# Kernel optimization log

Measured on AMD Instinct MI355X. Metric: run time of the kernel, lower is better.

## Reference

```python
import jax, jax.numpy as jnp
import numpy as np

B, N, F, D, H = 4, 2048, 128, 128, 4

def setup_inputs() -> dict:
    key = jax.random.key(0)
    k1, k2, k3, k4 = jax.random.split(key, 4)
    X = jax.random.normal(k1, (B, N, F), dtype=jnp.float32)
    A = jax.random.uniform(k2, (B, N, N), dtype=jnp.float32)
    kernel = jax.random.normal(k3, (F, D), dtype=jnp.float32) * 0.05
    bias = jnp.ones((D,), dtype=jnp.float32)
    attn = jax.random.normal(k4, (H, D, D), dtype=jnp.float32) * 0.05
    return {"X": X, "A": A, "kernel": kernel, "bias": bias, "attn": attn}

def reference(X, A, kernel, bias, attn):
    # Linear projection: [B,N,F] @ [F,D] + bias -> [B,N,D]
    Xp = jnp.einsum('bnf,fd->bnd', X, kernel) + bias
    # Per-head bilinear scores Xp @ attn_h @ Xp^T, batched over heads: [B,H,N,N]
    scores = jnp.einsum('bnd,hde,bme->bhnm', Xp, attn, Xp)
    # Adjacency mask + tanh (fused elementwise)
    Am = jnp.tanh(A[:, None, :, :] * scores)
    # Weighted aggregate per head: [B,H,N,N] @ [B,N,D] -> [B,H,N,D]
    heads = jnp.einsum('bhnm,bmd->bhnd', Am, Xp)
    # Mean over heads, relu
    Xh = jax.nn.relu(jnp.mean(heads, axis=1))
    # Skip connection (shapes match since F == D): relu(Xh + X)
    out = jax.nn.relu(Xh + X)
    return out
```

## Files before the change

### kernel.cpp

```cpp
#include <hip/hip_runtime.h>

#define NB 4
#define NN 2048
#define ND 128
#define NH 4

typedef short short8 __attribute__((ext_vector_type(8)));
typedef short short4v __attribute__((ext_vector_type(4)));
typedef float floatx4 __attribute__((ext_vector_type(4)));

__device__ __forceinline__ short f2bf(float f){
  unsigned u = __float_as_uint(f);
  u += 0x7FFFu + ((u >> 16) & 1u);
  return (short)(u >> 16);
}
__device__ __forceinline__ float bf2f(short s){
  unsigned u = ((unsigned)(unsigned short)s) << 16;
  return __uint_as_float(u);
}

__global__ void k0_transpose(const float* __restrict__ W, const float* __restrict__ attn,
                             short* __restrict__ WT, short* __restrict__ attnT){
  int mat = blockIdx.x;
  const float* src = (mat == 0) ? W : (attn + (mat - 1) * 16384);
  short* dst = (mat == 0) ? WT : (attnT + (mat - 1) * 16384);
  __shared__ short tile[128 * 130];
  int t = threadIdx.x;
  for (int k = 0; k < 64; ++k){
    int idx = k * 256 + t;
    int r = idx >> 7, c = idx & 127;
    tile[c * 130 + r] = f2bf(src[idx]);
  }
  __syncthreads();
  for (int k = 0; k < 8; ++k){
    int g = k * 256 + t;
    int r = g >> 4, c8 = g & 15;
    short8 v;
    #pragma unroll
    for (int j = 0; j < 8; ++j) v[j] = tile[r * 130 + c8 * 8 + j];
    *(short8*)&dst[r * 128 + c8 * 8] = v;
  }
}

__global__ __launch_bounds__(256) void k1_xp(const float* __restrict__ X,
                                             const short* __restrict__ WT,
                                             const float* __restrict__ bias,
                                             short* __restrict__ Xp){
  int bid = blockIdx.x;
  int b = bid >> 5, i0 = (bid & 31) << 6;
  int t = threadIdx.x, w = t >> 6, lane = t & 63, lq = lane >> 4, lc = lane & 15;
  __shared__ __align__(16) short ldsB[16384];
  #pragma unroll
  for (int c = 0; c < 8; ++c){
    int q = c * 256 + t; int fblk = q >> 7; int d = q & 127;
    *(short8*)&ldsB[q * 8] = *(const short8*)&WT[d * 128 + fblk * 8];
  }
  short8 af[4][4];
  #pragma unroll
  for (int ib = 0; ib < 4; ++ib)
    #pragma unroll
    for (int k = 0; k < 4; ++k){
      const float* xp = &X[(b * NN + i0 + ib * 16 + lc) * ND + k * 32 + lq * 8];
      float4 x0 = *(const float4*)xp;
      float4 x1 = *(const float4*)(xp + 4);
      short8 s;
      s[0]=f2bf(x0.x); s[1]=f2bf(x0.y); s[2]=f2bf(x0.z); s[3]=f2bf(x0.w);
      s[4]=f2bf(x1.x); s[5]=f2bf(x1.y); s[6]=f2bf(x1.z); s[7]=f2bf(x1.w);
      af[ib][k] = s;
    }
  __syncthreads();
  floatx4 acc[4][2];
  #pragma unroll
  for (int ib = 0; ib < 4; ++ib)
    #pragma unroll
    for (int eb = 0; eb < 2; ++eb) acc[ib][eb] = (floatx4){0.f, 0.f, 0.f, 0.f};
  #pragma unroll
  for (int eb = 0; eb < 2; ++eb)
    #pragma unroll
    for (int k = 0; k < 4; ++k){
      short8 bf = *(short8*)&ldsB[(k * 4 + lq) * 1024 + (w * 32 + eb * 16 + lc) * 8];
      #pragma unroll
      for (int ib = 0; ib < 4; ++ib)
        acc[ib][eb] = __builtin_amdgcn_mfma_f32_16x16x32_bf16(af[ib][k], bf, acc[ib][eb], 0, 0, 0);
    }
  #pragma unroll
  for (int ib = 0; ib < 4; ++ib)
    #pragma unroll
    for (int eb = 0; eb < 2; ++eb){
      int d = w * 32 + eb * 16 + lc;
      float bv = bias[d];
      #pragma unroll
      for (int r = 0; r < 4; ++r){
        int n = i0 + ib * 16 + lq * 4 + r;
        Xp[(b * NN + n) * ND + d] = f2bf(acc[ib][eb][r] + bv);
      }
    }
}

__global__ void k1b_transpose(const short* __restrict__ Xp, short* __restrict__ XpT){
  int bid = blockIdx.x;
  int b = bid >> 6; int rem = bid & 63;
  int n0 = (rem >> 1) << 6, d0 = (rem & 1) << 6;
  __shared__ short tile[64 * 66];
  int t = threadIdx.x;
  #pragma unroll
  for (int c = 0; c < 2; ++c){
    int g = c * 256 + t; int r = g >> 3, c8 = g & 7;
    short8 v = *(const short8*)&Xp[(b * NN + n0 + r) * ND + d0 + c8 * 8];
    #pragma unroll
    for (int j = 0; j < 8; ++j) tile[(c8 * 8 + j) * 66 + r] = v[j];
  }
  __syncthreads();
  #pragma unroll
  for (int c = 0; c < 2; ++c){
    int g = c * 256 + t; int d = g >> 3, n8 = g & 7;
    short8 v;
    #pragma unroll
    for (int j = 0; j < 8; ++j) v[j] = tile[d * 66 + n8 * 8 + j];
    *(short8*)&XpT[(b * ND + d0 + d) * NN + n0 + n8 * 8] = v;
  }
}

__global__ __launch_bounds__(256) void k2_y(const short* __restrict__ Xp,
                                            const short* __restrict__ attnT,
                                            short* __restrict__ Y){
  int bid = blockIdx.x;
  int it = bid & 31, h = (bid >> 5) & 3, b = bid >> 7;
  int i0 = it << 6;
  int t = threadIdx.x, w = t >> 6, lane = t & 63, lq = lane >> 4, lc = lane & 15;
  __shared__ __align__(16) short ldsB[16384];
  const short* Bsrc = attnT + h * 16384;
  #pragma unroll
  for (int c = 0; c < 8; ++c){
    int q = c * 256 + t; int dblk = q >> 7; int e = q & 127;
    *(short8*)&ldsB[q * 8] = *(const short8*)&Bsrc[e * 128 + dblk * 8];
  }
  short8 af[4][4];
  #pragma unroll
  for (int ib = 0; ib < 4; ++ib)
    #pragma unroll
    for (int k = 0; k < 4; ++k)
      af[ib][k] = *(const short8*)&Xp[(b * NN + i0 + ib * 16 + lc) * ND + k * 32 + lq * 8];
  __syncthreads();
  floatx4 acc[4][2];
  #pragma unroll
  for (int ib = 0; ib < 4; ++ib)
    #pragma unroll
    for (int eb = 0; eb < 2; ++eb) acc[ib][eb] = (floatx4){0.f, 0.f, 0.f, 0.f};
  #pragma unroll
  for (int eb = 0; eb < 2; ++eb)
    #pragma unroll
    for (int k = 0; k < 4; ++k){
      short8 bf = *(short8*)&ldsB[(k * 4 + lq) * 1024 + (w * 32 + eb * 16 + lc) * 8];
      #pragma unroll
      for (int ib = 0; ib < 4; ++ib)
        acc[ib][eb] = __builtin_amdgcn_mfma_f32_16x16x32_bf16(af[ib][k], bf, acc[ib][eb], 0, 0, 0);
    }
  #pragma unroll
  for (int ib = 0; ib < 4; ++ib)
    #pragma unroll
    for (int eb = 0; eb < 2; ++eb){
      int e = w * 32 + eb * 16 + lc;
      #pragma unroll
      for (int r = 0; r < 4; ++r){
        int n = i0 + ib * 16 + lq * 4 + r;
        Y[((b * NH + h) * NN + n) * ND + e] = f2bf(acc[ib][eb][r]);
      }
    }
}

__global__ __launch_bounds__(256, 3) void k3_fused(const short* __restrict__ Xp,
                                                   const short* __restrict__ XpT,
                                                   const short* __restrict__ Y,
                                                   const float* __restrict__ A,
                                                   float* __restrict__ part){
  int bid = blockIdx.x;
  int it = bid & 127, b = (bid >> 7) & 3, ms = bid >> 9;
  int i0 = it << 4;
  int t = threadIdx.x, w = t >> 6, lane = t & 63, lq = lane >> 4, lc = lane & 15;

  __shared__ __align__(16) short ldsPh[2][1024];
  __shared__ __align__(16) short ldsPl[2][1024];

  short8 yf[4][4];
  #pragma unroll
  for (int h = 0; h < 4; ++h)
    #pragma unroll
    for (int k = 0; k < 4; ++k)
      yf[h][k] = *(const short8*)&Y[((b * NH + h) * NN + i0 + lc) * ND + k * 32 + lq * 8];

  floatx4 acc[2];
  acc[0] = (floatx4){0.f,0.f,0.f,0.f};
  acc[1] = (floatx4){0.f,0.f,0.f,0.f};

  const int mbase = ms << 9;
  const int poff = (w * 2 + (lq >> 1)) * 128 + lc * 8 + (lq & 1) * 4;

  const short* xr  = Xp  + (size_t)(b * NN + mbase + w * 16 + lc) * ND;
  const short* pvB = XpT + (size_t)(b * ND + w * 32 + lc) * NN + mbase;
  const float* Ar  = A   + (size_t)(b * NN + i0 + lc) * NN + mbase + w * 16 + lq * 4;

  short8 xpf_c[4];
  #pragma unroll
  for (int k = 0; k < 4; ++k) xpf_c[k] = *(const short8*)&xr[k * 32 + lq * 8];
  floatx4 av_c = *(const floatx4*)Ar;

  for (int itn = 0; itn < 8; ++itn){
    int p = itn & 1;
    short8 pvb[2][2];
    #pragma unroll
    for (int kb = 0; kb < 2; ++kb)
      #pragma unroll
      for (int db = 0; db < 2; ++db)
        pvb[kb][db] = *(const short8*)&pvB[(size_t)(db * 16) * NN + kb * 32 + lq * 8];

    float av2[4];
    #pragma unroll
    for (int r = 0; r < 4; ++r) av2[r] = av_c[r] * 2.885390081777926f;
    float rs[4] = {0.f, 0.f, 0.f, 0.f};
    #pragma unroll
    for (int h = 0; h < 4; ++h){
      floatx4 S = (floatx4){0.f,0.f,0.f,0.f};
      #pragma unroll
      for (int k = 0; k < 4; ++k)
        S = __builtin_amdgcn_mfma_f32_16x16x32_bf16(xpf_c[k], yf[h][k], S, 0, 0, 0);
      #pragma unroll
      for (int r = 0; r < 4; ++r){
        float e = __builtin_amdgcn_exp2f(av2[r] * S[r]);
        rs[r] += __builtin_amdgcn_rcpf(e + 1.f);
      }
    }

    int adv = (itn < 7) ? 64 : 0;
    xr += (size_t)adv * ND; Ar += adv; 
    short8 xpf_n[4];
    #pragma unroll
    for (int k = 0; k < 4; ++k) xpf_n[k] = *(const short8*)&xr[k * 32 + lq * 8];
    floatx4 av_n = *(const floatx4*)Ar;

    short4v hi4, lo4;
    #pragma unroll
    for (int r = 0; r < 4; ++r){
      float pb = 1.f - 0.5f * rs[r];
      short h16 = f2bf(pb);
      hi4[r] = h16;
      lo4[r] = f2bf(pb - bf2f(h16));
    }
    *(short4v*)&ldsPh[p][poff] = hi4;
    *(short4v*)&ldsPl[p][poff] = lo4;

    asm volatile("s_waitcnt lgkmcnt(0)\n\ts_barrier" ::: "memory");

    #pragma unroll
    for (int kb = 0; kb < 2; ++kb){
      short8 ph = *(short8*)&ldsPh[p][(kb * 4 + lq) * 128 + lc * 8];
      short8 pl = *(short8*)&ldsPl[p][(kb * 4 + lq) * 128 + lc * 8];
      #pragma unroll
      for (int db = 0; db < 2; ++db){
        acc[db] = __builtin_amdgcn_mfma_f32_16x16x32_bf16(ph, pvb[kb][db], acc[db], 0, 0, 0);
        acc[db] = __builtin_amdgcn_mfma_f32_16x16x32_bf16(pl, pvb[kb][db], acc[db], 0, 0, 0);
      }
    }
    pvB += adv;
    #pragma unroll
    for (int k = 0; k < 4; ++k) xpf_c[k] = xpf_n[k];
    av_c = av_n;
  }
  float* dst = part + (size_t)ms * 1048576 + (b * NN + i0) * ND;
  #pragma unroll
  for (int db = 0; db < 2; ++db)
    #pragma unroll
    for (int r = 0; r < 4; ++r)
      dst[(lq * 4 + r) * ND + w * 32 + db * 16 + lc] = acc[db][r];
}

__global__ void k4_final(const float* __restrict__ part, const float* __restrict__ X,
                         float* __restrict__ out){
  int f = (blockIdx.x * 256 + threadIdx.x) * 4;
  float4 s0 = *(const float4*)(part + f);
  float4 s1 = *(const float4*)(part + 1048576 + f);
  float4 s2 = *(const float4*)(part + 2097152 + f);
  float4 s3 = *(const float4*)(part + 3145728 + f);
  float4 xv = *(const float4*)(X + f);
  float4 o;
  o.x = fmaxf(fmaxf(s0.x + s1.x + s2.x + s3.x, 0.f) + xv.x, 0.f);
  o.y = fmaxf(fmaxf(s0.y + s1.y + s2.y + s3.y, 0.f) + xv.y, 0.f);
  o.z = fmaxf(fmaxf(s0.z + s1.z + s2.z + s3.z, 0.f) + xv.z, 0.f);
  o.w = fmaxf(fmaxf(s0.w + s1.w + s2.w + s3.w, 0.f) + xv.w, 0.f);
  *(float4*)(out + f) = o;
}

extern "C" void kernel_launch(void* const* d_in, const int* in_sizes, int n_in,
                              void* d_out, int out_size, void* d_ws, size_t ws_size,
                              hipStream_t stream) {
  const float* X    = (const float*)d_in[0];
  const float* A    = (const float*)d_in[1];
  const float* W    = (const float*)d_in[2];
  const float* bias = (const float*)d_in[3];
  const float* attn = (const float*)d_in[4];
  float* out = (float*)d_out;

  const size_t OFF_XP    = 0;
  const size_t OFF_XPT   = (size_t)2 << 20;
  const size_t OFF_Y     = (size_t)4 << 20;
  const size_t OFF_PART  = (size_t)12 << 20;
  const size_t OFF_WT    = (size_t)28 << 20;
  const size_t OFF_ATTNT = OFF_WT + 32768;
  const size_t NEED = OFF_ATTNT + 131072;
  if (ws_size < NEED) return;

  char* ws = (char*)d_ws;
  short* Xp    = (short*)(ws + OFF_XP);
  short* XpT   = (short*)(ws + OFF_XPT);
  short* Y     = (short*)(ws + OFF_Y);
  float* part  = (float*)(ws + OFF_PART);
  short* WT    = (short*)(ws + OFF_WT);
  short* attnT = (short*)(ws + OFF_ATTNT);

  k0_transpose<<<5, 256, 0, stream>>>(W, attn, WT, attnT);
  k1_xp<<<128, 256, 0, stream>>>(X, WT, bias, Xp);
  k1b_transpose<<<256, 256, 0, stream>>>(Xp, XpT);
  k2_y<<<512, 256, 0, stream>>>(Xp, attnT, Y);
  k3_fused<<<2048, 256, 0, stream>>>(Xp, XpT, Y, A, part);
  k4_final<<<1024, 256, 0, stream>>>(part, X, out);
}
```

Measured before the change: 196.5 us.

## Fuse Xp transpose into projection; restructure aggregation with bpermute and per-wave full-D tiles

The projection kernel now stages its bias-added output in LDS and writes both Xp and its transpose, so the separate transpose launch goes away. The fused attention kernel now has each wave compute all 128 output columns for its own key slice. It shuffles the hi/lo bf16 probability fragments across lanes with ds_bpermute instead of LDS plus a per-iteration barrier. Wave partials are then reduced once through LDS at the end, and the M range is split in two instead of four, which halves the partial buffers read by the final kernel. In exchange, each thread holds more accumulator and B-fragment registers, which may lower occupancy, and half as many blocks are launched.

```diff
diff --git a/kernel.cpp b/kernel.cpp
--- a/kernel.cpp
+++ b/kernel.cpp
@@ -6,7 +6,6 @@
 #define NH 4
 
 typedef short short8 __attribute__((ext_vector_type(8)));
-typedef short short4v __attribute__((ext_vector_type(4)));
 typedef float floatx4 __attribute__((ext_vector_type(4)));
 
 __device__ __forceinline__ short f2bf(float f){
@@ -17,6 +16,9 @@
 __device__ __forceinline__ float bf2f(short s){
   unsigned u = ((unsigned)(unsigned short)s) << 16;
   return __uint_as_float(u);
+}
+__device__ __forceinline__ int pack2(short lo, short hi){
+  return ((int)(unsigned short)hi << 16) | (int)(unsigned short)lo;
 }
 
 __global__ void k0_transpose(const float* __restrict__ W, const float* __restrict__ attn,
@@ -45,7 +47,8 @@
 __global__ __launch_bounds__(256) void k1_xp(const float* __restrict__ X,
                                              const short* __restrict__ WT,
                                              const float* __restrict__ bias,
-                                             short* __restrict__ Xp){
+                                             short* __restrict__ Xp,
+                                             short* __restrict__ XpT){
   int bid = blockIdx.x;
   int b = bid >> 5, i0 = (bid & 31) << 6;
   int t = threadIdx.x, w = t >> 6, lane = t & 63, lq = lane >> 4, lc = lane & 15;
@@ -83,6 +86,7 @@
       for (int ib = 0; ib < 4; ++ib)
         acc[ib][eb] = __builtin_amdgcn_mfma_f32_16x16x32_bf16(af[ib][k], bf, acc[ib][eb], 0, 0, 0);
     }
+  __syncthreads();
   #pragma unroll
   for (int ib = 0; ib < 4; ++ib)
     #pragma unroll
@@ -91,33 +95,24 @@
       float bv = bias[d];
       #pragma unroll
       for (int r = 0; r < 4; ++r){
-        int n = i0 + ib * 16 + lq * 4 + r;
-        Xp[(b * NN + n) * ND + d] = f2bf(acc[ib][eb][r] + bv);
+        int n = ib * 16 + lq * 4 + r;
+        ldsB[d * 72 + n] = f2bf(acc[ib][eb][r] + bv);
       }
     }
-}
-
-__global__ void k1b_transpose(const short* __restrict__ Xp, short* __restrict__ XpT){
-  int bid = blockIdx.x;
-  int b = bid >> 6; int rem = bid & 63;
-  int n0 = (rem >> 1) << 6, d0 = (rem & 1) << 6;
-  __shared__ short tile[64 * 66];
-  int t = threadIdx.x;
-  #pragma unroll
-  for (int c = 0; c < 2; ++c){
-    int g = c * 256 + t; int r = g >> 3, c8 = g & 7;
-    short8 v = *(const short8*)&Xp[(b * NN + n0 + r) * ND + d0 + c8 * 8];
-    #pragma unroll
-    for (int j = 0; j < 8; ++j) tile[(c8 * 8 + j) * 66 + r] = v[j];
-  }
-  __syncthreads();
-  #pragma unroll
-  for (int c = 0; c < 2; ++c){
+  __syncthreads();
+  #pragma unroll
+  for (int c = 0; c < 4; ++c){
     int g = c * 256 + t; int d = g >> 3, n8 = g & 7;
+    short8 v = *(short8*)&ldsB[d * 72 + n8 * 8];
+    *(short8*)&XpT[(size_t)(b * ND + d) * NN + i0 + n8 * 8] = v;
+  }
+  #pragma unroll
+  for (int c = 0; c < 4; ++c){
+    int g = c * 256 + t; int n = g >> 4, d8 = g & 15;
     short8 v;
     #pragma unroll
-    for (int j = 0; j < 8; ++j) v[j] = tile[d * 66 + n8 * 8 + j];
-    *(short8*)&XpT[(b * ND + d0 + d) * NN + n0 + n8 * 8] = v;
+    for (int j = 0; j < 8; ++j) v[j] = ldsB[(d8 * 8 + j) * 72 + n];
+    *(short8*)&Xp[(size_t)(b * NN + i0 + n) * ND + d8 * 8] = v;
   }
 }
 
@@ -179,9 +174,6 @@
   int i0 = it << 4;
   int t = threadIdx.x, w = t >> 6, lane = t & 63, lq = lane >> 4, lc = lane & 15;
 
-  __shared__ __align__(16) short ldsPh[2][1024];
-  __shared__ __align__(16) short ldsPl[2][1024];
-
   short8 yf[4][4];
   #pragma unroll
   for (int h = 0; h < 4; ++h)
@@ -189,30 +181,28 @@
     for (int k = 0; k < 4; ++k)
       yf[h][k] = *(const short8*)&Y[((b * NH + h) * NN + i0 + lc) * ND + k * 32 + lq * 8];
 
-  floatx4 acc[2];
-  acc[0] = (floatx4){0.f,0.f,0.f,0.f};
-  acc[1] = (floatx4){0.f,0.f,0.f,0.f};
-
-  const int mbase = ms << 9;
-  const int poff = (w * 2 + (lq >> 1)) * 128 + lc * 8 + (lq & 1) * 4;
-
+  floatx4 acc[8];
+  #pragma unroll
+  for (int dt = 0; dt < 8; ++dt) acc[dt] = (floatx4){0.f,0.f,0.f,0.f};
+
+  const int mbase = ms << 10;
   const short* xr  = Xp  + (size_t)(b * NN + mbase + w * 16 + lc) * ND;
-  const short* pvB = XpT + (size_t)(b * ND + w * 32 + lc) * NN + mbase;
   const float* Ar  = A   + (size_t)(b * NN + i0 + lc) * NN + mbase + w * 16 + lq * 4;
+  const short* pvB = XpT + (size_t)(b * ND + lc) * NN + mbase + w * 16 + (lq & 1) * 8;
+  const int bpa0 = (((2 * lq) & 3) * 16 + lc) * 4;
+  const int bpa1 = bpa0 + 64;
+  const bool hih = (lq < 2);
 
   short8 xpf_c[4];
   #pragma unroll
   for (int k = 0; k < 4; ++k) xpf_c[k] = *(const short8*)&xr[k * 32 + lq * 8];
   floatx4 av_c = *(const floatx4*)Ar;
 
-  for (int itn = 0; itn < 8; ++itn){
-    int p = itn & 1;
-    short8 pvb[2][2];
-    #pragma unroll
-    for (int kb = 0; kb < 2; ++kb)
-      #pragma unroll
-      for (int db = 0; db < 2; ++db)
-        pvb[kb][db] = *(const short8*)&pvB[(size_t)(db * 16) * NN + kb * 32 + lq * 8];
+  for (int itn = 0; itn < 16; ++itn){
+    short8 pvb[8];
+    #pragma unroll
+    for (int dt = 0; dt < 8; ++dt)
+      pvb[dt] = *(const short8*)&pvB[(size_t)dt * 16 * NN];
 
     float av2[4];
     #pragma unroll
@@ -231,47 +221,67 @@
       }
     }
 
-    int adv = (itn < 7) ? 64 : 0;
-    xr += (size_t)adv * ND; Ar += adv; 
+    int adv = (itn < 15) ? 64 : 0;
+    xr += (size_t)adv * ND; Ar += adv;
     short8 xpf_n[4];
     #pragma unroll
     for (int k = 0; k < 4; ++k) xpf_n[k] = *(const short8*)&xr[k * 32 + lq * 8];
     floatx4 av_n = *(const floatx4*)Ar;
 
-    short4v hi4, lo4;
+    short hb[4], lb[4];
     #pragma unroll
     for (int r = 0; r < 4; ++r){
       float pb = 1.f - 0.5f * rs[r];
-      short h16 = f2bf(pb);
-      hi4[r] = h16;
-      lo4[r] = f2bf(pb - bf2f(h16));
-    }
-    *(short4v*)&ldsPh[p][poff] = hi4;
-    *(short4v*)&ldsPl[p][poff] = lo4;
-
-    asm volatile("s_waitcnt lgkmcnt(0)\n\ts_barrier" ::: "memory");
-
-    #pragma unroll
-    for (int kb = 0; kb < 2; ++kb){
-      short8 ph = *(short8*)&ldsPh[p][(kb * 4 + lq) * 128 + lc * 8];
-      short8 pl = *(short8*)&ldsPl[p][(kb * 4 + lq) * 128 + lc * 8];
-      #pragma unroll
-      for (int db = 0; db < 2; ++db){
-        acc[db] = __builtin_amdgcn_mfma_f32_16x16x32_bf16(ph, pvb[kb][db], acc[db], 0, 0, 0);
-        acc[db] = __builtin_amdgcn_mfma_f32_16x16x32_bf16(pl, pvb[kb][db], acc[db], 0, 0, 0);
-      }
-    }
+      hb[r] = f2bf(pb);
+      lb[r] = f2bf(pb - bf2f(hb[r]));
+    }
+    int ph0 = pack2(hb[0], hb[1]), ph1 = pack2(hb[2], hb[3]);
+    int pl0 = pack2(lb[0], lb[1]), pl1 = pack2(lb[2], lb[3]);
+
+    int h0 = __builtin_amdgcn_ds_bpermute(bpa0, ph0);
+    int l0 = __builtin_amdgcn_ds_bpermute(bpa0, pl0);
+    int h1 = __builtin_amdgcn_ds_bpermute(bpa0, ph1);
+    int l1 = __builtin_amdgcn_ds_bpermute(bpa0, pl1);
+    int h2 = __builtin_amdgcn_ds_bpermute(bpa1, ph0);
+    int l2 = __builtin_amdgcn_ds_bpermute(bpa1, pl0);
+    int h3 = __builtin_amdgcn_ds_bpermute(bpa1, ph1);
+    int l3 = __builtin_amdgcn_ds_bpermute(bpa1, pl1);
+    union { int4 i; short8 s; } cvt;
+    cvt.i.x = hih ? h0 : l0;
+    cvt.i.y = hih ? h1 : l1;
+    cvt.i.z = hih ? h2 : l2;
+    cvt.i.w = hih ? h3 : l3;
+    short8 pA = cvt.s;
+
+    #pragma unroll
+    for (int dt = 0; dt < 8; ++dt)
+      acc[dt] = __builtin_amdgcn_mfma_f32_16x16x32_bf16(pA, pvb[dt], acc[dt], 0, 0, 0);
+
     pvB += adv;
     #pragma unroll
     for (int k = 0; k < 4; ++k) xpf_c[k] = xpf_n[k];
     av_c = av_n;
   }
-  float* dst = part + (size_t)ms * 1048576 + (b * NN + i0) * ND;
-  #pragma unroll
-  for (int db = 0; db < 2; ++db)
+
+  __shared__ __align__(16) float red[4 * 2112];
+  float* myr = red + w * 2112;
+  #pragma unroll
+  for (int dt = 0; dt < 8; ++dt)
     #pragma unroll
     for (int r = 0; r < 4; ++r)
-      dst[(lq * 4 + r) * ND + w * 32 + db * 16 + lc] = acc[db][r];
+      myr[(lq * 4 + r) * 132 + dt * 16 + lc] = acc[dt][r];
+  __syncthreads();
+  int e0 = t * 8; int ii = e0 >> 7; int dd = e0 & 127;
+  int base = ii * 132 + dd;
+  floatx4 o0 = *(floatx4*)&red[base], o1 = *(floatx4*)&red[base + 4];
+  #pragma unroll
+  for (int wv = 1; wv < 4; ++wv){
+    o0 += *(floatx4*)&red[wv * 2112 + base];
+    o1 += *(floatx4*)&red[wv * 2112 + base + 4];
+  }
+  float* dst = part + (size_t)ms * 1048576 + (size_t)(b * NN + i0 + ii) * ND + dd;
+  *(floatx4*)dst = o0;
+  *(floatx4*)(dst + 4) = o1;
 }
 
 __global__ void k4_final(const float* __restrict__ part, const float* __restrict__ X,
@@ -279,14 +289,12 @@
   int f = (blockIdx.x * 256 + threadIdx.x) * 4;
   float4 s0 = *(const float4*)(part + f);
   float4 s1 = *(const float4*)(part + 1048576 + f);
-  float4 s2 = *(const float4*)(part + 2097152 + f);
-  float4 s3 = *(const float4*)(part + 3145728 + f);
   float4 xv = *(const float4*)(X + f);
   float4 o;
-  o.x = fmaxf(fmaxf(s0.x + s1.x + s2.x + s3.x, 0.f) + xv.x, 0.f);
-  o.y = fmaxf(fmaxf(s0.y + s1.y + s2.y + s3.y, 0.f) + xv.y, 0.f);
-  o.z = fmaxf(fmaxf(s0.z + s1.z + s2.z + s3.z, 0.f) + xv.z, 0.f);
-  o.w = fmaxf(fmaxf(s0.w + s1.w + s2.w + s3.w, 0.f) + xv.w, 0.f);
+  o.x = fmaxf(fmaxf(s0.x + s1.x, 0.f) + xv.x, 0.f);
+  o.y = fmaxf(fmaxf(s0.y + s1.y, 0.f) + xv.y, 0.f);
+  o.z = fmaxf(fmaxf(s0.z + s1.z, 0.f) + xv.z, 0.f);
+  o.w = fmaxf(fmaxf(s0.w + s1.w, 0.f) + xv.w, 0.f);
   *(float4*)(out + f) = o;
 }
 
@@ -304,7 +312,7 @@
   const size_t OFF_XPT   = (size_t)2 << 20;
   const size_t OFF_Y     = (size_t)4 << 20;
   const size_t OFF_PART  = (size_t)12 << 20;
-  const size_t OFF_WT    = (size_t)28 << 20;
+  const size_t OFF_WT    = (size_t)20 << 20;
   const size_t OFF_ATTNT = OFF_WT + 32768;
   const size_t NEED = OFF_ATTNT + 131072;
   if (ws_size < NEED) return;
@@ -318,9 +326,8 @@
   short* attnT = (short*)(ws + OFF_ATTNT);
 
   k0_transpose<<<5, 256, 0, stream>>>(W, attn, WT, attnT);
-  k1_xp<<<128, 256, 0, stream>>>(X, WT, bias, Xp);
-  k1b_transpose<<<256, 256, 0, stream>>>(Xp, XpT);
+  k1_xp<<<128, 256, 0, stream>>>(X, WT, bias, Xp, XpT);
   k2_y<<<512, 256, 0, stream>>>(Xp, attnT, Y);
-  k3_fused<<<2048, 256, 0, stream>>>(Xp, XpT, Y, A, part);
+  k3_fused<<<1024, 256, 0, stream>>>(Xp, XpT, Y, A, part);
   k4_final<<<1024, 256, 0, stream>>>(part, X, out);
 }
```

Result: slower. 230.1 us (+17.1%).
